# Performance work log

Measured on AMD Instinct MI355X. Metric: run time of the kernel, lower is better.

Reference implementation:

```python
import jax, jax.numpy as jnp
import numpy as np

B = 16384
IN_FEATURES = 256
OUT_FEATURES = 4096
CH_GROUP = 8
NUM_SLICE = IN_FEATURES // CH_GROUP  # 32


def setup_inputs() -> dict:
    key = jax.random.key(0)
    kx, kw = jax.random.split(key)
    x = jax.random.normal(kx, (B, IN_FEATURES), dtype=jnp.float32)
    # Stacked weights of the 32 tiny Linear(ch_group -> out_features, bias=False)
    # layers; W[i] corresponds to fc_i.weight with shape [out_features, ch_group].
    W = jax.random.normal(kw, (NUM_SLICE, OUT_FEATURES, CH_GROUP), dtype=jnp.float32) * (1.0 / np.sqrt(CH_GROUP))
    return {"x": x, "W": W}


def reference(x, W):
    # Equivalent to sum_i fc_i(x[:, i*cg:(i+1)*cg]) = fused block GEMM.
    xs = x.reshape(x.shape[0], NUM_SLICE, CH_GROUP)  # [B, S, C]
    # out[b,o] = sum_{s,c} xs[b,s,c] * W[s,o,c]
    return jnp.einsum('bsc,soc->bo', xs, W)
```

## Files before the change

kernel.cpp:

```cpp
#include <hip/hip_runtime.h>
#include <hip/hip_bf16.h>


typedef __attribute__((ext_vector_type(8)))  __bf16          bf16x8;
typedef __attribute__((ext_vector_type(8)))  unsigned short  ushort8;
typedef __attribute__((ext_vector_type(4)))  float           floatx4;

__device__ __forceinline__ unsigned short f2bf(float f) {
    union { float f; unsigned u; } v; v.f = f;
    unsigned r = v.u + 0x7fffu + ((v.u >> 16) & 1u);
    return (unsigned short)(r >> 16);
}

__global__ void conv_x_kernel(const float* __restrict__ x,
                              unsigned short* __restrict__ xb) {
    const int t = blockIdx.x * 256 + threadIdx.x;
    const float4* p = (const float4*)x;
    float4 a = p[2 * t], b = p[2 * t + 1];
    ushort8 v;
    v[0] = f2bf(a.x); v[1] = f2bf(a.y); v[2] = f2bf(a.z); v[3] = f2bf(a.w);
    v[4] = f2bf(b.x); v[5] = f2bf(b.y); v[6] = f2bf(b.z); v[7] = f2bf(b.w);
    *(ushort8*)(xb + (size_t)t * 8) = v;
}

__global__ void pack_w_kernel(const float* __restrict__ W,
                              unsigned short* __restrict__ wb) {
    const int t = blockIdx.x * 256 + threadIdx.x;
    const int s = t >> 12;
    const int o = t & 4095;
    const float4* p = (const float4*)(W + (size_t)s * 32768 + (size_t)o * 8);
    float4 a = p[0], b = p[1];
    ushort8 v;
    v[0] = f2bf(a.x); v[1] = f2bf(a.y); v[2] = f2bf(a.z); v[3] = f2bf(a.w);
    v[4] = f2bf(b.x); v[5] = f2bf(b.y); v[6] = f2bf(b.z); v[7] = f2bf(b.w);
    *(ushort8*)(wb + (size_t)o * 256 + (size_t)s * 8) = v;
}

__device__ __forceinline__ void gload_lds16(const unsigned short* g, unsigned short* l) {
    __builtin_amdgcn_global_load_lds(
        (const __attribute__((address_space(1))) unsigned int*)(const void*)g,
        (__attribute__((address_space(3))) unsigned int*)(void*)l,
        16, 0, 0);
}

__device__ __forceinline__ void stage_tile(const unsigned short* Ag,
                                           const unsigned short* Bg,
                                           unsigned short* la,
                                           unsigned short* lb) {
#pragma unroll
    for (int j = 0; j < 4; ++j) {
        gload_lds16(Ag + j * 32 * 256, la + j * 32 * 64);
        gload_lds16(Bg + j * 32 * 256, lb + j * 32 * 64);
    }
}

__global__ __launch_bounds__(256) void gemm_kernel(
    const unsigned short* __restrict__ A,
    const unsigned short* __restrict__ Bt,
    float* __restrict__ C) {
    __shared__ __align__(16) unsigned short lsA[2][128 * 64];
    __shared__ __align__(16) unsigned short lsB[2][128 * 64];

    const int tid  = threadIdx.x;
    const int wave = tid >> 6;
    const int lane = tid & 63;
    const int bm   = blockIdx.y;
    const int bn   = blockIdx.x;

    const int srow = wave * 8 + (lane >> 3);
    const int gchunk = (lane & 7) ^ ((lane >> 3) & 7);
    const unsigned short* Ag = A  + ((size_t)(bm * 128 + srow)) * 256 + gchunk * 8;
    const unsigned short* Bg = Bt + ((size_t)(bn * 128 + srow)) * 256 + gchunk * 8;
    unsigned short* laW0 = &lsA[0][wave * 512];
    unsigned short* lbW0 = &lsB[0][wave * 512];
    unsigned short* laW1 = &lsA[1][wave * 512];
    unsigned short* lbW1 = &lsB[1][wave * 512];

    const int wrow = wave >> 1, wcol = wave & 1;
    const int fr = lane & 15;
    const int fq = lane >> 4;
    const int fsw = fr & 7;
    const unsigned short* aB = &lsA[0][(wrow * 64 + fr) * 64];
    const unsigned short* bB = &lsB[0][(wcol * 64 + fr) * 64];
    const int bufStride = 128 * 64;

    floatx4 acc[4][4] = {};

    stage_tile(Ag, Bg, laW0, lbW0);
    __syncthreads();

    int cur = 0;
#pragma unroll
    for (int kt = 0; kt < 4; ++kt) {
        if (kt < 3) {
            const int ko = (kt + 1) * 64;
            if (cur == 0) stage_tile(Ag + ko, Bg + ko, laW1, lbW1);
            else          stage_tile(Ag + ko, Bg + ko, laW0, lbW0);
        }

        const unsigned short* aT = aB + cur * bufStride;
        const unsigned short* bT = bB + cur * bufStride;
#pragma unroll
        for (int ks = 0; ks < 2; ++ks) {
            const int so = ((ks * 4 + fq) ^ fsw) * 8;
            bf16x8 af[4], bv[4];
#pragma unroll
            for (int i = 0; i < 4; ++i) {
                af[i] = *(const bf16x8*)(const void*)(aT + i * 1024 + so);
                bv[i] = *(const bf16x8*)(const void*)(bT + i * 1024 + so);
            }
#pragma unroll
            for (int j = 0; j < 4; ++j)
#pragma unroll
                for (int i = 0; i < 4; ++i)
                    acc[j][i] = __builtin_amdgcn_mfma_f32_16x16x32_bf16(
                        bv[j], af[i], acc[j][i], 0, 0, 0);
        }
        __syncthreads();
        cur ^= 1;
    }

    const int row0 = bm * 128 + wrow * 64 + fr;
    const int col0 = bn * 128 + wcol * 64 + fq * 4;
#pragma unroll
    for (int i = 0; i < 4; ++i) {
        float* Cp = C + (size_t)(row0 + i * 16) * 4096 + col0;
#pragma unroll
        for (int j = 0; j < 4; ++j)
            *(floatx4*)(Cp + j * 16) = acc[j][i];
    }
}

extern "C" void kernel_launch(void* const* d_in, const int* in_sizes, int n_in,
                              void* d_out, int out_size, void* d_ws, size_t ws_size,
                              hipStream_t stream) {
    const float* x = (const float*)d_in[0];
    const float* W = (const float*)d_in[1];
    float* out = (float*)d_out;

    unsigned short* xb = (unsigned short*)d_ws;
    unsigned short* wb = xb + (size_t)16384 * 256;

    conv_x_kernel<<<2048, 256, 0, stream>>>(x, xb);
    pack_w_kernel<<<512, 256, 0, stream>>>(W, wb);

    dim3 grid(32, 128);
    gemm_kernel<<<grid, 256, 0, stream>>>(xb, wb, out);
}
```

Baseline: 312.3 us.

## Merge prep kernels, halve K-tile for occupancy, remap blocks, nontemporal stores

The x-conversion and W-packing kernels become a single launch. The GEMM K tile shrinks from 64 to 32, which halves LDS use and with launch_bounds(256,4) allows more blocks per CU; it now runs 8 double-buffered K steps with a new swizzle. Block IDs are remapped so neighbouring blocks are spread across the grid for XCD/L2 locality, and output stores become nontemporal to avoid polluting cache with the 256MB fp32 output. In exchange there are more barriers per tile, and the launch bound may constrain registers.

```diff
diff --git a/kernel.cpp b/kernel.cpp
--- a/kernel.cpp
+++ b/kernel.cpp
@@ -12,28 +12,29 @@
     return (unsigned short)(r >> 16);
 }
 
-__global__ void conv_x_kernel(const float* __restrict__ x,
-                              unsigned short* __restrict__ xb) {
-    const int t = blockIdx.x * 256 + threadIdx.x;
-    const float4* p = (const float4*)x;
-    float4 a = p[2 * t], b = p[2 * t + 1];
-    ushort8 v;
-    v[0] = f2bf(a.x); v[1] = f2bf(a.y); v[2] = f2bf(a.z); v[3] = f2bf(a.w);
-    v[4] = f2bf(b.x); v[5] = f2bf(b.y); v[6] = f2bf(b.z); v[7] = f2bf(b.w);
-    *(ushort8*)(xb + (size_t)t * 8) = v;
-}
-
-__global__ void pack_w_kernel(const float* __restrict__ W,
-                              unsigned short* __restrict__ wb) {
-    const int t = blockIdx.x * 256 + threadIdx.x;
-    const int s = t >> 12;
-    const int o = t & 4095;
-    const float4* p = (const float4*)(W + (size_t)s * 32768 + (size_t)o * 8);
-    float4 a = p[0], b = p[1];
-    ushort8 v;
-    v[0] = f2bf(a.x); v[1] = f2bf(a.y); v[2] = f2bf(a.z); v[3] = f2bf(a.w);
-    v[4] = f2bf(b.x); v[5] = f2bf(b.y); v[6] = f2bf(b.z); v[7] = f2bf(b.w);
-    *(ushort8*)(wb + (size_t)o * 256 + (size_t)s * 8) = v;
+__global__ __launch_bounds__(256) void prep_kernel(
+    const float* __restrict__ x, const float* __restrict__ W,
+    unsigned short* __restrict__ xb, unsigned short* __restrict__ wb) {
+    const int b = blockIdx.x;
+    if (b < 2048) {
+        const int t = b * 256 + threadIdx.x;
+        const float4* p = (const float4*)x;
+        float4 a = p[2 * t], c = p[2 * t + 1];
+        ushort8 v;
+        v[0] = f2bf(a.x); v[1] = f2bf(a.y); v[2] = f2bf(a.z); v[3] = f2bf(a.w);
+        v[4] = f2bf(c.x); v[5] = f2bf(c.y); v[6] = f2bf(c.z); v[7] = f2bf(c.w);
+        *(ushort8*)(xb + (size_t)t * 8) = v;
+    } else {
+        const int t = (b - 2048) * 256 + threadIdx.x;
+        const int s = t >> 12;
+        const int o = t & 4095;
+        const float4* p = (const float4*)(W + (size_t)s * 32768 + (size_t)o * 8);
+        float4 a = p[0], c = p[1];
+        ushort8 v;
+        v[0] = f2bf(a.x); v[1] = f2bf(a.y); v[2] = f2bf(a.z); v[3] = f2bf(a.w);
+        v[4] = f2bf(c.x); v[5] = f2bf(c.y); v[6] = f2bf(c.z); v[7] = f2bf(c.w);
+        *(ushort8*)(wb + (size_t)o * 256 + (size_t)s * 8) = v;
+    }
 }
 
 __device__ __forceinline__ void gload_lds16(const unsigned short* g, unsigned short* l) {
@@ -43,81 +44,70 @@
         16, 0, 0);
 }
 
-__device__ __forceinline__ void stage_tile(const unsigned short* Ag,
-                                           const unsigned short* Bg,
-                                           unsigned short* la,
-                                           unsigned short* lb) {
-#pragma unroll
-    for (int j = 0; j < 4; ++j) {
-        gload_lds16(Ag + j * 32 * 256, la + j * 32 * 64);
-        gload_lds16(Bg + j * 32 * 256, lb + j * 32 * 64);
-    }
-}
-
-__global__ __launch_bounds__(256) void gemm_kernel(
+__global__ __launch_bounds__(256, 4) void gemm_kernel(
     const unsigned short* __restrict__ A,
     const unsigned short* __restrict__ Bt,
     float* __restrict__ C) {
-    __shared__ __align__(16) unsigned short lsA[2][128 * 64];
-    __shared__ __align__(16) unsigned short lsB[2][128 * 64];
+    __shared__ __align__(16) unsigned short lsA[2][128 * 32];
+    __shared__ __align__(16) unsigned short lsB[2][128 * 32];
 
     const int tid  = threadIdx.x;
     const int wave = tid >> 6;
     const int lane = tid & 63;
-    const int bm   = blockIdx.y;
-    const int bn   = blockIdx.x;
 
-    const int srow = wave * 8 + (lane >> 3);
-    const int gchunk = (lane & 7) ^ ((lane >> 3) & 7);
-    const unsigned short* Ag = A  + ((size_t)(bm * 128 + srow)) * 256 + gchunk * 8;
-    const unsigned short* Bg = Bt + ((size_t)(bn * 128 + srow)) * 256 + gchunk * 8;
-    unsigned short* laW0 = &lsA[0][wave * 512];
-    unsigned short* lbW0 = &lsB[0][wave * 512];
-    unsigned short* laW1 = &lsA[1][wave * 512];
-    unsigned short* lbW1 = &lsB[1][wave * 512];
+    const int flat = blockIdx.y * 32 + blockIdx.x;
+    const int nid  = (flat & 7) * 512 + (flat >> 3);
+    const int bm   = nid >> 5;
+    const int bn   = nid & 31;
+
+    const int sr  = tid >> 2;
+    const int gch = (tid & 3) ^ ((tid >> 3) & 3);
+    const unsigned short* Ag = A  + ((size_t)(bm * 128 + sr)) * 256 + gch * 8;
+    const unsigned short* Bg = Bt + ((size_t)(bn * 128 + sr)) * 256 + gch * 8;
+    unsigned short* laW[2] = { &lsA[0][wave * 512], &lsA[1][wave * 512] };
+    unsigned short* lbW[2] = { &lsB[0][wave * 512], &lsB[1][wave * 512] };
 
     const int wrow = wave >> 1, wcol = wave & 1;
     const int fr = lane & 15;
     const int fq = lane >> 4;
-    const int fsw = fr & 7;
-    const unsigned short* aB = &lsA[0][(wrow * 64 + fr) * 64];
-    const unsigned short* bB = &lsB[0][(wcol * 64 + fr) * 64];
-    const int bufStride = 128 * 64;
+    const int so = (fq ^ ((fr >> 1) & 3)) * 8;
+    const unsigned short* aF[2] = { &lsA[0][(wrow * 64 + fr) * 32] + so,
+                                    &lsA[1][(wrow * 64 + fr) * 32] + so };
+    const unsigned short* bF[2] = { &lsB[0][(wcol * 64 + fr) * 32] + so,
+                                    &lsB[1][(wcol * 64 + fr) * 32] + so };
 
     floatx4 acc[4][4] = {};
 
-    stage_tile(Ag, Bg, laW0, lbW0);
+    gload_lds16(Ag,            laW[0]);
+    gload_lds16(Ag + 64 * 256, laW[0] + 2048);
+    gload_lds16(Bg,            lbW[0]);
+    gload_lds16(Bg + 64 * 256, lbW[0] + 2048);
     __syncthreads();
 
-    int cur = 0;
 #pragma unroll
-    for (int kt = 0; kt < 4; ++kt) {
-        if (kt < 3) {
-            const int ko = (kt + 1) * 64;
-            if (cur == 0) stage_tile(Ag + ko, Bg + ko, laW1, lbW1);
-            else          stage_tile(Ag + ko, Bg + ko, laW0, lbW0);
+    for (int kt = 0; kt < 8; ++kt) {
+        const int cur = kt & 1;
+        if (kt < 7) {
+            const int ko = (kt + 1) * 32;
+            gload_lds16(Ag + ko,            laW[cur ^ 1]);
+            gload_lds16(Ag + ko + 64 * 256, laW[cur ^ 1] + 2048);
+            gload_lds16(Bg + ko,            lbW[cur ^ 1]);
+            gload_lds16(Bg + ko + 64 * 256, lbW[cur ^ 1] + 2048);
         }
 
-        const unsigned short* aT = aB + cur * bufStride;
-        const unsigned short* bT = bB + cur * bufStride;
+        bf16x8 af[4], bv[4];
 #pragma unroll
-        for (int ks = 0; ks < 2; ++ks) {
-            const int so = ((ks * 4 + fq) ^ fsw) * 8;
-            bf16x8 af[4], bv[4];
+        for (int i = 0; i < 4; ++i) {
+            af[i] = *(const bf16x8*)(const void*)(aF[cur] + i * 512);
+            bv[i] = *(const bf16x8*)(const void*)(bF[cur] + i * 512);
+        }
 #pragma unroll
-            for (int i = 0; i < 4; ++i) {
-                af[i] = *(const bf16x8*)(const void*)(aT + i * 1024 + so);
-                bv[i] = *(const bf16x8*)(const void*)(bT + i * 1024 + so);
-            }
+        for (int j = 0; j < 4; ++j)
 #pragma unroll
-            for (int j = 0; j < 4; ++j)
-#pragma unroll
-                for (int i = 0; i < 4; ++i)
-                    acc[j][i] = __builtin_amdgcn_mfma_f32_16x16x32_bf16(
-                        bv[j], af[i], acc[j][i], 0, 0, 0);
-        }
+            for (int i = 0; i < 4; ++i)
+                acc[j][i] = __builtin_amdgcn_mfma_f32_16x16x32_bf16(
+                    bv[j], af[i], acc[j][i], 0, 0, 0);
         __syncthreads();
-        cur ^= 1;
     }
 
     const int row0 = bm * 128 + wrow * 64 + fr;
@@ -127,7 +117,7 @@
         float* Cp = C + (size_t)(row0 + i * 16) * 4096 + col0;
 #pragma unroll
         for (int j = 0; j < 4; ++j)
-            *(floatx4*)(Cp + j * 16) = acc[j][i];
+            __builtin_nontemporal_store(acc[j][i], (floatx4*)(Cp + j * 16));
     }
 }
 
@@ -141,8 +131,7 @@
     unsigned short* xb = (unsigned short*)d_ws;
     unsigned short* wb = xb + (size_t)16384 * 256;
 
-    conv_x_kernel<<<2048, 256, 0, stream>>>(x, xb);
-    pack_w_kernel<<<512, 256, 0, stream>>>(W, wb);
+    prep_kernel<<<2560, 256, 0, stream>>>(x, W, xb, wb);
 
     dim3 grid(32, 128);
     gemm_kernel<<<grid, 256, 0, stream>>>(xb, wb, out);
```

After: 312.7 us. Within noise of the previous version (+0.1%).
